# Kernel optimization log

Measured on AMD Instinct MI355X. Metric: run time of the kernel, lower is better.

## Reference

```python
import jax, jax.numpy as jnp
import numpy as np

THRESHOLD = 0.4
TOPK = 4


def _box_iou(boxes1, boxes2):
    # boxes1: [B, Q, 4], boxes2: [B, G, 4] in (x1, y1, x2, y2)
    area1 = (boxes1[..., 2] - boxes1[..., 0]) * (boxes1[..., 3] - boxes1[..., 1])  # [B,Q]
    area2 = (boxes2[..., 2] - boxes2[..., 0]) * (boxes2[..., 3] - boxes2[..., 1])  # [B,G]
    lt = jnp.maximum(boxes1[:, :, None, :2], boxes2[:, None, :, :2])  # [B,Q,G,2]
    rb = jnp.minimum(boxes1[:, :, None, 2:], boxes2[:, None, :, 2:])  # [B,Q,G,2]
    wh = jnp.clip(rb - lt, 0.0)
    inter = wh[..., 0] * wh[..., 1]                                   # [B,Q,G]
    union = area1[:, :, None] + area2[:, None, :] - inter
    return inter / (union + 1e-07)


def _make_boxes(key, b, n):
    k1, k2 = jax.random.split(key)
    xy = jax.random.uniform(k1, (b, n, 2), dtype=jnp.float32) * 0.8
    wh = jax.random.uniform(k2, (b, n, 2), dtype=jnp.float32) * 0.2 + 0.01
    return jnp.concatenate([xy, xy + wh], axis=-1)  # valid x1<x2, y1<y2


def setup_inputs() -> dict:
    key = jax.random.key(0)
    k1, k2, k3 = jax.random.split(key, 3)
    B, Q, G = 128, 1000, 300
    pred_logits = jax.random.normal(k1, (B, Q, 1), dtype=jnp.float32)
    pred_boxes_xyxy = _make_boxes(k2, B, Q)
    tgt_boxes_xyxy = _make_boxes(k3, B, G)
    return {
        "pred_logits": pred_logits,
        "pred_boxes_xyxy": pred_boxes_xyxy,
        "tgt_boxes_xyxy": tgt_boxes_xyxy,
    }


def reference(pred_logits, pred_boxes_xyxy, tgt_boxes_xyxy):
    # Per-query binary score.
    score = jax.nn.sigmoid(pred_logits)[..., 0]              # [B,Q]
    iou = _box_iou(pred_boxes_xyxy, tgt_boxes_xyxy)          # [B,Q,G]
    valid = (iou > THRESHOLD).astype(score.dtype)
    gt_score = score[:, :, None] * iou * valid               # [B,Q,G]
    # Per-GT top-k over queries (same matches as the nested-loop original:
    # invalid entries are zero, and positives-only are kept via the mask).
    vals, idxs = jax.lax.top_k(jnp.swapaxes(gt_score, 1, 2), TOPK)  # [B,G,K]
    mask = vals > 0.0                                        # valid match mask
    return vals, idxs.astype(jnp.int32), mask
```

## Files before the change

kernel.cpp:

```cpp
#include <hip/hip_runtime.h>

#define NB 128
#define NQ 1000
#define NG 300
#define NK 4
#define THRESH 0.4f

#define GCHUNKS 4
#define GPERB   (NG / GCHUNKS)
#define CAP     40

__global__ __launch_bounds__(1024) void fused_matcher(
    const float* __restrict__ logits,
    const float* __restrict__ pboxes,
    const float* __restrict__ tboxes,
    float* __restrict__ out_vals,
    float* __restrict__ out_idx,
    float* __restrict__ out_mask)
{
    __shared__ float4 spb[1024];
    __shared__ float  sscore[1024];
    __shared__ float4 stb[GPERB];
    __shared__ float  sta[GPERB];
    __shared__ unsigned scnt[GPERB];
    __shared__ unsigned short sslot[GPERB][CAP];

    const int b   = blockIdx.y;
    const int gc  = blockIdx.x;
    const int tid = threadIdx.x;
    const int g0  = gc * GPERB;

    float4 p;
    float  s = 0.0f;
    if (tid < NQ) {
        p = reinterpret_cast<const float4*>(pboxes)[(size_t)b * NQ + tid];
        float x = logits[(size_t)b * NQ + tid];
        s = 1.0f / (1.0f + expf(-x));
    } else {
        p = make_float4(2e9f, 2e9f, 2e9f, 2e9f);
    }
    spb[tid]    = p;
    sscore[tid] = s;
    const float pa999 = 0.999f * ((p.z - p.x) * (p.w - p.y));

    if (tid < GPERB) {
        float4 t = reinterpret_cast<const float4*>(tboxes)[(size_t)b * NG + g0 + tid];
        stb[tid]  = t;
        sta[tid]  = 0.999f * ((t.z - t.x) * (t.w - t.y));
        scnt[tid] = 0u;
    }
    __syncthreads();

#pragma unroll 5
    for (int gi = 0; gi < GPERB; ++gi) {
        const float4 tb = stb[gi];
        const float  ta = sta[gi];

        float ltx = fmaxf(p.x, tb.x);
        float lty = fmaxf(p.y, tb.y);
        float rbx = fminf(p.z, tb.z);
        float rby = fminf(p.w, tb.w);
        float w = fmaxf(rbx - ltx, 0.0f);
        float h = fmaxf(rby - lty, 0.0f);
        float inter = w * h;

        if (fmaf(inter, 3.5f, -pa999) >= ta) {
            unsigned pos = atomicAdd(&scnt[gi], 1u);
            if (pos < CAP) sslot[gi][pos] = (unsigned short)tid;
        }
    }
    __syncthreads();

    if (tid < GPERB) {
        const float4 tb = stb[tid];
        const float tarea = (tb.z - tb.x) * (tb.w - tb.y);
        int n = (int)scnt[tid];
        if (n > CAP) n = CAP;

        unsigned long long k0 = 0ull, k1 = 0ull, k2 = 0ull, k3 = 0ull;
        for (int i = 0; i < n; ++i) {
            const int q = sslot[tid][i];
            const float4 pp = spb[q];
            float parea = (pp.z - pp.x) * (pp.w - pp.y);
            float ltx = fmaxf(pp.x, tb.x);
            float lty = fmaxf(pp.y, tb.y);
            float rbx = fminf(pp.z, tb.z);
            float rby = fminf(pp.w, tb.w);
            float w = fmaxf(rbx - ltx, 0.0f);
            float h = fmaxf(rby - lty, 0.0f);
            float inter = w * h;
            float uni   = parea + tarea - inter;
            float iou   = inter / (uni + 1e-7f);
            if (iou > THRESH) {
                float val = sscore[q] * iou;
                unsigned long long ck =
                    ((unsigned long long)__float_as_uint(val) << 32) |
                    (unsigned long long)(unsigned)(~(unsigned)q);
                if (ck > k3) {
                    if (ck > k0)      { k3 = k2; k2 = k1; k1 = k0; k0 = ck; }
                    else if (ck > k1) { k3 = k2; k2 = k1; k1 = ck; }
                    else if (ck > k2) { k3 = k2; k2 = ck; }
                    else              { k3 = ck; }
                }
            }
        }

        const int iq0 = k0 ? (int)~(unsigned)k0 : -1;
        const int iq1 = k1 ? (int)~(unsigned)k1 : -1;
        const int iq2 = k2 ? (int)~(unsigned)k2 : -1;
        float4 vv, vi, vm;
        float* pv = &vv.x; float* pi_ = &vi.x; float* pm = &vm.x;
        int fill = 0;
        unsigned long long ks[1];
#define EMIT(J, KJ)                                                         \
        {                                                                   \
            if (KJ != 0ull) {                                               \
                pv[J]  = __uint_as_float((unsigned)(KJ >> 32));             \
                pi_[J] = (float)(int)~(unsigned)KJ;                         \
                pm[J]  = 1.0f;                                              \
            } else {                                                        \
                while (fill == iq0 || fill == iq1 || fill == iq2) ++fill;   \
                pv[J]  = 0.0f;                                              \
                pi_[J] = (float)fill;                                       \
                pm[J]  = 0.0f;                                              \
                ++fill;                                                     \
            }                                                               \
        }
        EMIT(0, k0) EMIT(1, k1) EMIT(2, k2) EMIT(3, k3)
#undef EMIT
        (void)ks;
        const size_t o4 = (size_t)b * NG + g0 + tid;
        reinterpret_cast<float4*>(out_vals)[o4] = vv;
        reinterpret_cast<float4*>(out_idx)[o4]  = vi;
        reinterpret_cast<float4*>(out_mask)[o4] = vm;
    }
}

extern "C" void kernel_launch(void* const* d_in, const int* in_sizes, int n_in,
                              void* d_out, int out_size, void* d_ws, size_t ws_size,
                              hipStream_t stream) {
    const float* logits = (const float*)d_in[0];
    const float* pboxes = (const float*)d_in[1];
    const float* tboxes = (const float*)d_in[2];

    float* out = (float*)d_out;
    const size_t bgk = (size_t)NB * NG * NK;
    float* out_vals = out;
    float* out_idx  = out + bgk;
    float* out_mask = out + 2 * bgk;

    dim3 grid(GCHUNKS, NB);
    fused_matcher<<<grid, 1024, 0, stream>>>(logits, pboxes, tboxes,
                                             out_vals, out_idx, out_mask);
}
```

Baseline: 28.15 us.

## Split per-GT top-4 selection across 8 lanes with shuffle merge; read target boxes from global

The final top-k phase now gives each GT box 8 threads instead of 1. Each thread scans a strided subset of candidate queries, and the per-thread top-4 lists are combined with a bitonic-style shuffle merge over three xor steps. This targets the serial tail where only 75 threads did all the candidate scanning. The change also drops the shared-memory copy of the target boxes and reads them straight from global memory (uniform loads) in the IoU loop, which may add global-memory latency to the main loop.

```diff
diff --git a/kernel.cpp b/kernel.cpp
--- a/kernel.cpp
+++ b/kernel.cpp
@@ -20,7 +20,6 @@
 {
     __shared__ float4 spb[1024];
     __shared__ float  sscore[1024];
-    __shared__ float4 stb[GPERB];
     __shared__ float  sta[GPERB];
     __shared__ unsigned scnt[GPERB];
     __shared__ unsigned short sslot[GPERB][CAP];
@@ -29,6 +28,9 @@
     const int gc  = blockIdx.x;
     const int tid = threadIdx.x;
     const int g0  = gc * GPERB;
+
+    const float4* __restrict__ tb4 =
+        reinterpret_cast<const float4*>(tboxes) + (size_t)b * NG + g0;
 
     float4 p;
     float  s = 0.0f;
@@ -44,8 +46,7 @@
     const float pa999 = 0.999f * ((p.z - p.x) * (p.w - p.y));
 
     if (tid < GPERB) {
-        float4 t = reinterpret_cast<const float4*>(tboxes)[(size_t)b * NG + g0 + tid];
-        stb[tid]  = t;
+        float4 t = tb4[tid];
         sta[tid]  = 0.999f * ((t.z - t.x) * (t.w - t.y));
         scnt[tid] = 0u;
     }
@@ -53,7 +54,7 @@
 
 #pragma unroll 5
     for (int gi = 0; gi < GPERB; ++gi) {
-        const float4 tb = stb[gi];
+        const float4 tb = tb4[gi];
         const float  ta = sta[gi];
 
         float ltx = fmaxf(p.x, tb.x);
@@ -71,15 +72,17 @@
     }
     __syncthreads();
 
-    if (tid < GPERB) {
-        const float4 tb = stb[tid];
+    const int grp = tid >> 3;
+    const int l8  = tid & 7;
+    if (grp < GPERB) {
+        const float4 tb = tb4[grp];
         const float tarea = (tb.z - tb.x) * (tb.w - tb.y);
-        int n = (int)scnt[tid];
+        int n = (int)scnt[grp];
         if (n > CAP) n = CAP;
 
         unsigned long long k0 = 0ull, k1 = 0ull, k2 = 0ull, k3 = 0ull;
-        for (int i = 0; i < n; ++i) {
-            const int q = sslot[tid][i];
+        for (int i = l8; i < n; i += 8) {
+            const int q = sslot[grp][i];
             const float4 pp = spb[q];
             float parea = (pp.z - pp.x) * (pp.w - pp.y);
             float ltx = fmaxf(pp.x, tb.x);
@@ -105,34 +108,56 @@
             }
         }
 
-        const int iq0 = k0 ? (int)~(unsigned)k0 : -1;
-        const int iq1 = k1 ? (int)~(unsigned)k1 : -1;
-        const int iq2 = k2 ? (int)~(unsigned)k2 : -1;
-        float4 vv, vi, vm;
-        float* pv = &vv.x; float* pi_ = &vi.x; float* pm = &vm.x;
-        int fill = 0;
-        unsigned long long ks[1];
+#define MERGE_STEP(MASK)                                                    \
+        {                                                                   \
+            unsigned long long p0 = __shfl_xor(k0, MASK, 64);               \
+            unsigned long long p1 = __shfl_xor(k1, MASK, 64);               \
+            unsigned long long p2 = __shfl_xor(k2, MASK, 64);               \
+            unsigned long long p3 = __shfl_xor(k3, MASK, 64);               \
+            k0 = k0 > p3 ? k0 : p3;                                         \
+            k1 = k1 > p2 ? k1 : p2;                                         \
+            k2 = k2 > p1 ? k2 : p1;                                         \
+            k3 = k3 > p0 ? k3 : p0;                                         \
+            unsigned long long t;                                           \
+            if (k0 < k2) { t = k0; k0 = k2; k2 = t; }                       \
+            if (k1 < k3) { t = k1; k1 = k3; k3 = t; }                       \
+            if (k0 < k1) { t = k0; k0 = k1; k1 = t; }                       \
+            if (k2 < k3) { t = k2; k2 = k3; k3 = t; }                       \
+        }
+        MERGE_STEP(1)
+        MERGE_STEP(2)
+        MERGE_STEP(4)
+#undef MERGE_STEP
+
+        if (l8 == 0) {
+            const int iq0 = k0 ? (int)~(unsigned)k0 : -1;
+            const int iq1 = k1 ? (int)~(unsigned)k1 : -1;
+            const int iq2 = k2 ? (int)~(unsigned)k2 : -1;
+            float4 vv, vi, vm;
+            float* pv = &vv.x; float* pi_ = &vi.x; float* pm = &vm.x;
+            int fill = 0;
 #define EMIT(J, KJ)                                                         \
-        {                                                                   \
-            if (KJ != 0ull) {                                               \
-                pv[J]  = __uint_as_float((unsigned)(KJ >> 32));             \
-                pi_[J] = (float)(int)~(unsigned)KJ;                         \
-                pm[J]  = 1.0f;                                              \
-            } else {                                                        \
-                while (fill == iq0 || fill == iq1 || fill == iq2) ++fill;   \
-                pv[J]  = 0.0f;                                              \
-                pi_[J] = (float)fill;                                       \
-                pm[J]  = 0.0f;                                              \
-                ++fill;                                                     \
-            }                                                               \
+            {                                                               \
+                if (KJ != 0ull) {                                           \
+                    pv[J]  = __uint_as_float((unsigned)(KJ >> 32));         \
+                    pi_[J] = (float)(int)~(unsigned)KJ;                     \
+                    pm[J]  = 1.0f;                                          \
+                } else {                                                    \
+                    while (fill == iq0 || fill == iq1 || fill == iq2)       \
+                        ++fill;                                             \
+                    pv[J]  = 0.0f;                                          \
+                    pi_[J] = (float)fill;                                   \
+                    pm[J]  = 0.0f;                                          \
+                    ++fill;                                                 \
+                }                                                           \
+            }
+            EMIT(0, k0) EMIT(1, k1) EMIT(2, k2) EMIT(3, k3)
+#undef EMIT
+            const size_t o4 = (size_t)b * NG + g0 + grp;
+            reinterpret_cast<float4*>(out_vals)[o4] = vv;
+            reinterpret_cast<float4*>(out_idx)[o4]  = vi;
+            reinterpret_cast<float4*>(out_mask)[o4] = vm;
         }
-        EMIT(0, k0) EMIT(1, k1) EMIT(2, k2) EMIT(3, k3)
-#undef EMIT
-        (void)ks;
-        const size_t o4 = (size_t)b * NG + g0 + tid;
-        reinterpret_cast<float4*>(out_vals)[o4] = vv;
-        reinterpret_cast<float4*>(out_idx)[o4]  = vi;
-        reinterpret_cast<float4*>(out_mask)[o4] = vm;
     }
 }
 
```

Result: slower. 63.67 us (+126.2%).
